# Kernel tuning notes

Hardware: AMD Instinct MI355X
Metric: run time of the kernel (lower is better)

The kernel has to match this reference:

```python
import jax, jax.numpy as jnp
import numpy as np

T, B, D, H, F, E = 2048, 2, 1024, 16, 4096, 8
HD = D // H


def layer_norm(x, g, b, eps=1e-5):
    m = x.mean(-1, keepdims=True)
    v = ((x - m) ** 2).mean(-1, keepdims=True)
    return (x - m) * jax.lax.rsqrt(v + eps) * g + b


def setup_inputs() -> dict:
    key = jax.random.key(0)
    ks = jax.random.split(key, 24)
    s = 0.02
    inp = {
        "x": jax.random.normal(ks[0], (T, B, D), jnp.float32),
        # self-attention (fairseq MultiheadAttention)
        "Wq": jax.random.normal(ks[1], (D, D), jnp.float32) * s,
        "bq": jnp.zeros((D,), jnp.float32),
        "Wk": jax.random.normal(ks[2], (D, D), jnp.float32) * s,
        "bk": jnp.zeros((D,), jnp.float32),
        "Wv": jax.random.normal(ks[3], (D, D), jnp.float32) * s,
        "bv": jnp.zeros((D,), jnp.float32),
        "Wo": jax.random.normal(ks[4], (D, D), jnp.float32) * s,
        "bo": jnp.zeros((D,), jnp.float32),
        "ln1_g": jnp.ones((D,), jnp.float32),
        "ln1_b": jnp.zeros((D,), jnp.float32),
        "ln2_g": jnp.ones((D,), jnp.float32),
        "ln2_b": jnp.zeros((D,), jnp.float32),
        # MoE: expert_centroids Linear(D -> E, bias=False) => weight [E, D]
        "cent": jax.random.normal(ks[5], (E, D), jnp.float32) * s,
        # per-expert MoESublayer params (base_sublayers=1)
        "e_ln_g": jnp.ones((E, D), jnp.float32),
        "e_ln_b": jnp.zeros((E, D), jnp.float32),
        "e_W1": jax.random.normal(ks[6], (E, D, F), jnp.float32) * s,
        "e_b1": jnp.zeros((E, F), jnp.float32),
        "e_W2": jax.random.normal(ks[7], (E, F, D), jnp.float32) * s,
        "e_b2": jnp.zeros((E, D), jnp.float32),
    }
    return inp


def reference(x, Wq, bq, Wk, bk, Wv, bv, Wo, bo, ln1_g, ln1_b, ln2_g, ln2_b,
              cent, e_ln_g, e_ln_b, e_W1, e_b1, e_W2, e_b2):
    # ---- self-attention block (pre-norm, causal) ----
    res = x  # [T,B,D]
    h = layer_norm(x, ln1_g, ln1_b)
    q = ((h @ Wq) + bq) * (HD ** -0.5)
    k = h @ Wk + bk
    v = h @ Wv + bv
    q = q.reshape(T, B, H, HD)
    k = k.reshape(T, B, H, HD)
    v = v.reshape(T, B, H, HD)
    scores = jnp.einsum('tbhd,sbhd->bhts', q, k)
    causal = jnp.tril(jnp.ones((T, T), bool))
    scores = jnp.where(causal, scores, -1e9)
    p = jax.nn.softmax(scores, axis=-1)
    a = jnp.einsum('bhts,sbhd->tbhd', p, v).reshape(T, B, D)
    x = res + (a @ Wo + bo)

    # ---- MoE block (pre-norm) ----
    res = x
    h = layer_norm(x, ln2_g, ln2_b)
    # MoELayer: transpose(0,1) then flatten -> [B*T, D] token-major by batch
    xs = h.transpose(1, 0, 2).reshape(B * T, D)
    logits = xs.astype(jnp.float32) @ cent.T  # fp32 gating, [N,E]
    assign = jnp.argmax(logits, axis=-1)      # greedy top-1 routing

    # single-device semantics: All2All identity; sort + inverse-sort cancel,
    # so out[t] = expert_{assign[t]}(xs[t]). Compute each expert densely and select.
    def sublayer(g, b, W1, b1, W2, b2):
        hh = jax.nn.relu(layer_norm(xs, g, b) @ W1 + b1)  # [N,F]
        return xs + hh @ W2 + b2                          # internal residual

    ys = jax.vmap(sublayer)(e_ln_g, e_ln_b, e_W1, e_b1, e_W2, e_b2)  # [E,N,D]
    moe_out = jnp.take_along_axis(ys, assign[None, :, None], axis=0)[0]  # [N,D]
    moe_out = moe_out.reshape(B, T, D).transpose(1, 0, 2)  # back to [T,B,D]

    return res + moe_out
```

## Files before the change

kernel.cpp:

```cpp
#include <hip/hip_runtime.h>
#include <hip/hip_bf16.h>
#include <math.h>

#define T_ 2048
#define B_ 2
#define D_ 1024
#define H_ 16
#define F_ 4096
#define E_ 8
#define N_ 4096
#define HD_ 64
#define PADROWS 5120

typedef __attribute__((ext_vector_type(8))) short short8_t;
typedef __attribute__((ext_vector_type(4))) float f32x4_t;
typedef __attribute__((ext_vector_type(16))) float f32x16_t;
typedef __attribute__((ext_vector_type(4))) unsigned u32x4_t;

__device__ __forceinline__ unsigned short f2bf(float f) {
    union { float f; unsigned u; } a; a.f = f;
    unsigned r = a.u + 0x7FFFu + ((a.u >> 16) & 1u);
    return (unsigned short)(r >> 16);
}

__device__ __forceinline__ unsigned cvtpk(float lo, float hi) {
    unsigned r;
    asm("v_cvt_pk_bf16_f32 %0, %1, %2" : "=v"(r) : "v"(lo), "v"(hi));
    return r;
}

__device__ __forceinline__ void glds16(const unsigned short* g, unsigned short* l) {
    __builtin_amdgcn_global_load_lds(
        (const __attribute__((address_space(1))) void*)g,
        (__attribute__((address_space(3))) void*)l, 16, 0, 0);
}

__device__ __forceinline__ void blockReduce2(float& a, float& b, float* sm) {
    #pragma unroll
    for (int m = 32; m; m >>= 1) { a += __shfl_xor(a, m); b += __shfl_xor(b, m); }
    const int w = threadIdx.x >> 6, l = threadIdx.x & 63;
    __syncthreads();
    if (l == 0) { sm[w] = a; sm[8 + w] = b; }
    __syncthreads();
    a = sm[0] + sm[1] + sm[2] + sm[3];
    b = sm[8] + sm[9] + sm[10] + sm[11];
}

__global__ __launch_bounds__(256) void k_transpose(const float* __restrict__ in,
                                                   unsigned short* __restrict__ out,
                                                   int R, int C) {
    __shared__ float tile[32][33];
    const int c0 = blockIdx.x * 32, r0 = blockIdx.y * 32;
    const size_t base = (size_t)blockIdx.z * R * C;
    in += base; out += base;
    const int tx = threadIdx.x & 31, ty = threadIdx.x >> 5;
    #pragma unroll
    for (int i = 0; i < 32; i += 8)
        tile[ty + i][tx] = in[(size_t)(r0 + ty + i) * C + c0 + tx];
    __syncthreads();
    #pragma unroll
    for (int i = 0; i < 32; i += 8)
        out[(size_t)(c0 + ty + i) * R + r0 + tx] = f2bf(tile[tx][ty + i]);
}

__global__ __launch_bounds__(256) void k_transpose_v(const unsigned short* __restrict__ in,
                                                     unsigned short* __restrict__ out) {
    const int bh = blockIdx.x;
    const int t0 = blockIdx.y * 128;
    const int tid = threadIdx.x;
    const int hd = tid & 63;
    const size_t ib = (size_t)bh * T_ * HD_;
    const size_t ob = (size_t)bh * HD_ * T_;
    for (int tb = tid >> 6; tb < 16; tb += 4) {
        const int t = t0 + tb * 8;
        short8_t v;
        #pragma unroll
        for (int k = 0; k < 8; ++k)
            v[k] = (short)in[ib + (size_t)(t + k) * HD_ + hd];
        *(short8_t*)(out + ob + (size_t)hd * T_ + t) = v;
    }
}

__global__ __launch_bounds__(256) void k_ln(const float* __restrict__ x,
                                            const float* __restrict__ g,
                                            const float* __restrict__ b,
                                            unsigned short* __restrict__ out) {
    __shared__ float sm[16];
    const int row = blockIdx.x, tid = threadIdx.x;
    const float4 v = *(const float4*)(x + (size_t)row * D_ + tid * 4);
    float s1 = v.x + v.y + v.z + v.w;
    float s2 = v.x * v.x + v.y * v.y + v.z * v.z + v.w * v.w;
    blockReduce2(s1, s2, sm);
    const float mean = s1 * (1.f / D_);
    const float inv  = rsqrtf(s2 * (1.f / D_) - mean * mean + 1e-5f);
    const float4 gg = *(const float4*)(g + tid * 4);
    const float4 bb = *(const float4*)(b + tid * 4);
    unsigned long long pk =
          (unsigned long long)f2bf((v.x - mean) * inv * gg.x + bb.x)
        | ((unsigned long long)f2bf((v.y - mean) * inv * gg.y + bb.y) << 16)
        | ((unsigned long long)f2bf((v.z - mean) * inv * gg.z + bb.z) << 32)
        | ((unsigned long long)f2bf((v.w - mean) * inv * gg.w + bb.w) << 48);
    *(unsigned long long*)(out + (size_t)row * D_ + tid * 4) = pk;
}

__device__ __forceinline__ void gemm_core(const unsigned short* ap0, const unsigned short* ap1,
                                          const unsigned short* bp0, const unsigned short* bp1,
                                          int K, unsigned short* Als, unsigned short* Bls,
                                          f32x4_t (&acc)[4][4]) {
    const int tid = threadIdx.x, w = tid >> 6, l = tid & 63;
    const int wm = (w >> 1) * 64, wn = (w & 1) * 64;
    const int fr = l & 15, fg = (l >> 4) * 8;
    f32x4_t z4 = {0.f, 0.f, 0.f, 0.f};
    #pragma unroll
    for (int m = 0; m < 4; m++)
        #pragma unroll
        for (int n = 0; n < 4; n++) acc[m][n] = z4;
    glds16(ap0, Als + w * 512);
    glds16(ap1, Als + (w + 4) * 512);
    glds16(bp0, Bls + w * 512);
    glds16(bp1, Bls + (w + 4) * 512);
    ap0 += 32; ap1 += 32; bp0 += 32; bp1 += 32;
    asm volatile("s_waitcnt vmcnt(0)" ::: "memory");
    __syncthreads();
    const int nk = K >> 5;
    #pragma unroll 2
    for (int kt = 0; kt < nk; ++kt) {
        const unsigned cur = (kt & 1) ? 4096u : 0u;
        const unsigned nxt = cur ^ 4096u;
        if (kt + 1 < nk) {
            glds16(ap0, Als + nxt + w * 512);
            glds16(ap1, Als + nxt + (w + 4) * 512);
            glds16(bp0, Bls + nxt + w * 512);
            glds16(bp1, Bls + nxt + (w + 4) * 512);
            ap0 += 32; ap1 += 32; bp0 += 32; bp1 += 32;
        }
        short8_t a[4], b[4];
        #pragma unroll
        for (int m = 0; m < 4; m++) a[m] = *(const short8_t*)(Als + cur + (wm + m * 16 + fr) * 32 + fg);
        #pragma unroll
        for (int n = 0; n < 4; n++) b[n] = *(const short8_t*)(Bls + cur + (wn + n * 16 + fr) * 32 + fg);
        #pragma unroll
        for (int m = 0; m < 4; m++)
            #pragma unroll
            for (int n = 0; n < 4; n++)
                acc[m][n] = __builtin_amdgcn_mfma_f32_16x16x32_bf16(a[m], b[n], acc[m][n], 0, 0, 0);
        __syncthreads();
    }
}

__global__ __launch_bounds__(256) void k_gemm_qkv(
    const unsigned short* __restrict__ A, const unsigned short* __restrict__ BT,
    const float* __restrict__ bq, const float* __restrict__ bk, const float* __restrict__ bv,
    unsigned short* __restrict__ Qb, unsigned short* __restrict__ Kb, unsigned short* __restrict__ Vb) {
    __shared__ unsigned short Als[8192], Bls[8192];
    const int tid = threadIdx.x, w = tid >> 6, l = tid & 63;
    const int col0 = blockIdx.x * 128, row0 = blockIdx.y * 128;
    const int r0s = w * 16 + (l >> 2), r1s = 64 + w * 16 + (l >> 2), cs = (l & 3) * 8;
    const unsigned short* ap0 = A + (size_t)(row0 + r0s) * D_ + cs;
    const unsigned short* ap1 = A + (size_t)(row0 + r1s) * D_ + cs;
    const unsigned short* bp0 = BT + (size_t)(col0 + r0s) * D_ + cs;
    const unsigned short* bp1 = BT + (size_t)(col0 + r1s) * D_ + cs;
    f32x4_t acc[4][4];
    gemm_core(ap0, ap1, bp0, bp1, D_, Als, Bls, acc);
    const int wm = (w >> 1) * 64, wn = (w & 1) * 64, fr = l & 15, fg4 = l >> 4;
    #pragma unroll
    for (int n = 0; n < 4; n++) {
        const int gcol = col0 + wn + n * 16 + fr;
        const int which = gcol >> 10, dc = gcol & 1023;
        const float bias = which == 0 ? bq[dc] : (which == 1 ? bk[dc] : bv[dc]);
        unsigned short* dst = which == 0 ? Qb : (which == 1 ? Kb : Vb);
        const int hh = dc >> 6, hd = dc & 63;
        #pragma unroll
        for (int m = 0; m < 4; m++)
            #pragma unroll
            for (int rr = 0; rr < 4; rr++) {
                const int grow = row0 + wm + m * 16 + fg4 * 4 + rr;
                float v = acc[m][n][rr] + bias;
                if (which == 0) v *= 0.1803368801111204f;
                const int t = grow >> 1, bb = grow & 1;
                dst[((size_t)(bb * H_ + hh) * T_ + t) * HD_ + hd] = f2bf(v);
            }
    }
}

__global__ __launch_bounds__(256) void k_attn(const unsigned short* __restrict__ Qb,
                                              const unsigned short* __restrict__ Kb,
                                              const unsigned short* __restrict__ Vt,
                                              unsigned short* __restrict__ aout) {
    __shared__ unsigned short Kl[2][4096];
    __shared__ unsigned short Vl[2][4096];
    const int id = blockIdx.x;
    const int qt = (id < 256) ? (15 - (id & 15)) : (id & 15);
    const int bh = (id >> 4) & 31;
    const int tid = threadIdx.x, w = tid >> 6, l = tid & 63;
    const int q5 = l & 31, hi = l >> 5, l7 = l & 7;
    const int row0 = w * 8 + (l >> 3);
    const int swz = ((l & 7) ^ (l >> 3)) * 8;
    const size_t base = (size_t)bh * T_ * HD_;
    const unsigned short* Qp = Qb + base;
    const unsigned short* kps = Kb + base + (size_t)row0 * HD_ + swz;
    const unsigned short* vps = Vt + base + (size_t)row0 * T_ + swz;
    const int qw0 = qt * 128 + w * 32;
    const int q = qw0 + q5;

    short8_t aq[4];
    #pragma unroll
    for (int khd = 0; khd < 4; ++khd)
        aq[khd] = *(const short8_t*)(Qp + (size_t)q * HD_ + khd * 16 + hi * 8);

    f32x16_t accO0, accO1;
    #pragma unroll
    for (int i = 0; i < 16; ++i) { accO0[i] = 0.f; accO1[i] = 0.f; }
    float mrun = -1e30f, lrun = 0.f;

    const int niter = (qt + 1) * 2;

    glds16(kps,            &Kl[0][w * 512]);
    glds16(kps + 32 * HD_, &Kl[0][2048 + w * 512]);
    glds16(vps,            &Vl[0][w * 512]);
    glds16(vps + 32 * T_,  &Vl[0][2048 + w * 512]);
    asm volatile("s_waitcnt vmcnt(0)" ::: "memory");
    __syncthreads();

    for (int it = 0; it < niter; ++it) {
        const int cur = it & 1;
        const int s0 = it * 64;
        if (it + 1 < niter) {
            const size_t ko = (size_t)(it + 1) * 64 * HD_;
            const int vo = (it + 1) * 64;
            glds16(kps + ko,            &Kl[cur ^ 1][w * 512]);
            glds16(kps + ko + 32 * HD_, &Kl[cur ^ 1][2048 + w * 512]);
            glds16(vps + vo,            &Vl[cur ^ 1][w * 512]);
            glds16(vps + vo + 32 * T_,  &Vl[cur ^ 1][2048 + w * 512]);
        }
        if (s0 <= qw0 + 31) {
            const unsigned short* KT = Kl[cur];
            const unsigned short* VT = Vl[cur];

            f32x16_t st0, st1;
            #pragma unroll
            for (int i = 0; i < 16; ++i) { st0[i] = 0.f; st1[i] = 0.f; }
            #pragma unroll
            for (int khd = 0; khd < 4; ++khd) {
                const int cb = (khd * 16 + hi * 8) ^ (l7 * 8);
                const short8_t k0 = *(const short8_t*)(KT + q5 * 64 + cb);
                const short8_t k1 = *(const short8_t*)(KT + (32 + q5) * 64 + cb);
                st0 = __builtin_amdgcn_mfma_f32_32x32x16_bf16(k0, aq[khd], st0, 0, 0, 0);
                st1 = __builtin_amdgcn_mfma_f32_32x32x16_bf16(k1, aq[khd], st1, 0, 0, 0);
            }

            const bool domask = (s0 + 63 > qw0);
            float pmax = -3e38f;
            #pragma unroll
            for (int r = 0; r < 16; ++r) {
                float v0 = st0[r], v1 = st1[r];
                if (domask) {
                    const int kv0 = s0 + (r & 3) + 8 * (r >> 2) + 4 * hi;
                    if (kv0 > q)      v0 = -1e30f;
                    if (kv0 + 32 > q) v1 = -1e30f;
                }
                st0[r] = v0; st1[r] = v1;
                pmax = fmaxf(pmax, fmaxf(v0, v1));
            }
            pmax = fmaxf(pmax, __shfl_xor(pmax, 32));
            const float mnew = fmaxf(mrun, pmax);
            const float scl = exp2f(mrun - mnew);
            float pt0[16], pt1[16];
            float rs = 0.f;
            #pragma unroll
            for (int r = 0; r < 16; ++r) {
                pt0[r] = exp2f(st0[r] - mnew);
                pt1[r] = exp2f(st1[r] - mnew);
                rs += pt0[r] + pt1[r];
            }
            rs += __shfl_xor(rs, 32);
            lrun = lrun * scl + rs;
            mrun = mnew;
            #pragma unroll
            for (int i = 0; i < 16; ++i) { accO0[i] *= scl; accO1[i] *= scl; }

            unsigned Wp[2][4][2];
            #pragma unroll
            for (int b = 0; b < 4; ++b) {
                Wp[0][b][0] = cvtpk(pt0[4 * b + 0], pt0[4 * b + 1]);
                Wp[0][b][1] = cvtpk(pt0[4 * b + 2], pt0[4 * b + 3]);
                Wp[1][b][0] = cvtpk(pt1[4 * b + 0], pt1[4 * b + 1]);
                Wp[1][b][1] = cvtpk(pt1[4 * b + 2], pt1[4 * b + 3]);
            }

            #pragma unroll
            for (int ks = 0; ks < 4; ++ks) {
                const int t = ks >> 1, b0 = (ks & 1) * 2;
                const unsigned ownA0 = Wp[t][b0][0],     ownA1 = Wp[t][b0][1];
                const unsigned ownB0 = Wp[t][b0 + 1][0], ownB1 = Wp[t][b0 + 1][1];
                const unsigned send0 = hi ? ownA0 : ownB0;
                const unsigned send1 = hi ? ownA1 : ownB1;
                const unsigned recv0 = __shfl_xor(send0, 32);
                const unsigned recv1 = __shfl_xor(send1, 32);
                u32x4_t wds;
                wds[0] = hi ? recv0 : ownA0;
                wds[1] = hi ? recv1 : ownA1;
                wds[2] = hi ? ownB0 : recv0;
                wds[3] = hi ? ownB1 : recv1;
                const short8_t pfrag = __builtin_bit_cast(short8_t, wds);
                const int cb = (ks * 16 + hi * 8) ^ (l7 * 8);
                const short8_t v0 = *(const short8_t*)(VT + q5 * 64 + cb);
                const short8_t v1 = *(const short8_t*)(VT + (32 + q5) * 64 + cb);
                accO0 = __builtin_amdgcn_mfma_f32_32x32x16_bf16(v0, pfrag, accO0, 0, 0, 0);
                accO1 = __builtin_amdgcn_mfma_f32_32x32x16_bf16(v1, pfrag, accO1, 0, 0, 0);
            }
        }
        asm volatile("s_waitcnt vmcnt(0)" ::: "memory");
        __syncthreads();
    }

    const float linv = 1.f / lrun;
    const int bidx = bh >> 4, hidx = bh & 15;
    unsigned short* orow = aout + (size_t)(q * B_ + bidx) * D_ + hidx * 64;
    #pragma unroll
    for (int g = 0; g < 4; ++g) {
        const int hd0 = 8 * g + 4 * hi;
        unsigned long long pk0 =
              (unsigned long long)f2bf(accO0[4 * g + 0] * linv)
            | ((unsigned long long)f2bf(accO0[4 * g + 1] * linv) << 16)
            | ((unsigned long long)f2bf(accO0[4 * g + 2] * linv) << 32)
            | ((unsigned long long)f2bf(accO0[4 * g + 3] * linv) << 48);
        *(unsigned long long*)(orow + hd0) = pk0;
        unsigned long long pk1 =
              (unsigned long long)f2bf(accO1[4 * g + 0] * linv)
            | ((unsigned long long)f2bf(accO1[4 * g + 1] * linv) << 16)
            | ((unsigned long long)f2bf(accO1[4 * g + 2] * linv) << 32)
            | ((unsigned long long)f2bf(accO1[4 * g + 3] * linv) << 48);
        *(unsigned long long*)(orow + 32 + hd0) = pk1;
    }
}

__global__ __launch_bounds__(256) void k_gemm_o(
    const unsigned short* __restrict__ A, const unsigned short* __restrict__ BT,
    const float* __restrict__ bo, const float* __restrict__ xin, float* __restrict__ x2) {
    __shared__ unsigned short Als[8192], Bls[8192];
    const int tid = threadIdx.x, w = tid >> 6, l = tid & 63;
    const int col0 = blockIdx.x * 128, row0 = blockIdx.y * 128;
    const int r0s = w * 16 + (l >> 2), r1s = 64 + w * 16 + (l >> 2), cs = (l & 3) * 8;
    const unsigned short* ap0 = A + (size_t)(row0 + r0s) * D_ + cs;
    const unsigned short* ap1 = A + (size_t)(row0 + r1s) * D_ + cs;
    const unsigned short* bp0 = BT + (size_t)(col0 + r0s) * D_ + cs;
    const unsigned short* bp1 = BT + (size_t)(col0 + r1s) * D_ + cs;
    f32x4_t acc[4][4];
    gemm_core(ap0, ap1, bp0, bp1, D_, Als, Bls, acc);
    const int wm = (w >> 1) * 64, wn = (w & 1) * 64, fr = l & 15, fg4 = l >> 4;
    #pragma unroll
    for (int n = 0; n < 4; n++) {
        const int gcol = col0 + wn + n * 16 + fr;
        const float bias = bo[gcol];
        #pragma unroll
        for (int m = 0; m < 4; m++)
            #pragma unroll
            for (int rr = 0; rr < 4; rr++) {
                const int grow = row0 + wm + m * 16 + fg4 * 4 + rr;
                const size_t idx = (size_t)grow * D_ + gcol;
                x2[idx] = xin[idx] + acc[m][n][rr] + bias;
            }
    }
}

__global__ __launch_bounds__(256) void k_ln2_gate(
    float* __restrict__ x2, const float* __restrict__ g2, const float* __restrict__ b2,
    const float* __restrict__ cent, const float* __restrict__ eg, const float* __restrict__ eb,
    unsigned short* __restrict__ z, int* __restrict__ assign, int* __restrict__ counts) {
    __shared__ float sm[48];
    const int row = blockIdx.x, tid = threadIdx.x;
    const int w = tid >> 6, l = tid & 63;
    float* xr = x2 + (size_t)row * D_;
    const float4 v = *(const float4*)(xr + tid * 4);
    float s1 = v.x + v.y + v.z + v.w;
    float s2 = v.x * v.x + v.y * v.y + v.z * v.z + v.w * v.w;
    blockReduce2(s1, s2, sm);
    const float mean = s1 * (1.f / D_);
    const float inv  = rsqrtf(s2 * (1.f / D_) - mean * mean + 1e-5f);
    const float4 gg = *(const float4*)(g2 + tid * 4), bb = *(const float4*)(b2 + tid * 4);
    float4 u;
    u.x = (v.x - mean) * inv * gg.x + bb.x;
    u.y = (v.y - mean) * inv * gg.y + bb.y;
    u.z = (v.z - mean) * inv * gg.z + bb.z;
    u.w = (v.w - mean) * inv * gg.w + bb.w;
    float p[E_];
    #pragma unroll
    for (int e = 0; e < E_; e++) {
        const float4 c = *(const float4*)(cent + (size_t)e * D_ + tid * 4);
        p[e] = u.x * c.x + u.y * c.y + u.z * c.z + u.w * c.w;
    }
    #pragma unroll
    for (int m = 32; m; m >>= 1)
        #pragma unroll
        for (int e = 0; e < E_; e++) p[e] += __shfl_xor(p[e], m);
    __syncthreads();
    if (l == 0) {
        #pragma unroll
        for (int e = 0; e < E_; e++) sm[16 + e * 4 + w] = p[e];
    }
    __syncthreads();
    int best = 0; float bl = -1e30f;
    #pragma unroll
    for (int e = 0; e < E_; e++) {
        const float le = sm[16 + e * 4] + sm[16 + e * 4 + 1] + sm[16 + e * 4 + 2] + sm[16 + e * 4 + 3];
        if (le > bl) { bl = le; best = e; }
    }
    float t1 = u.x + u.y + u.z + u.w;
    float t2 = u.x * u.x + u.y * u.y + u.z * u.z + u.w * u.w;
    blockReduce2(t1, t2, sm);
    const float m2   = t1 * (1.f / D_);
    const float inv2 = rsqrtf(t2 * (1.f / D_) - m2 * m2 + 1e-5f);
    const float4 egv = *(const float4*)(eg + (size_t)best * D_ + tid * 4);
    const float4 ebv = *(const float4*)(eb + (size_t)best * D_ + tid * 4);
    unsigned long long pk =
          (unsigned long long)f2bf((u.x - m2) * inv2 * egv.x + ebv.x)
        | ((unsigned long long)f2bf((u.y - m2) * inv2 * egv.y + ebv.y) << 16)
        | ((unsigned long long)f2bf((u.z - m2) * inv2 * egv.z + ebv.z) << 32)
        | ((unsigned long long)f2bf((u.w - m2) * inv2 * egv.w + ebv.w) << 48);
    *(unsigned long long*)(z + (size_t)row * D_ + tid * 4) = pk;
    float4 xu; xu.x = v.x + u.x; xu.y = v.y + u.y; xu.z = v.z + u.z; xu.w = v.w + u.w;
    *(float4*)(xr + tid * 4) = xu;
    if (tid == 0) { assign[row] = best; atomicAdd(&counts[best], 1); }
}

__global__ void k_init(int* counts, int* cursor, int* perm) {
    const int t = threadIdx.x;
    if (t < E_) { counts[t] = 0; cursor[t] = 0; }
    for (int i = t; i < PADROWS; i += 256) perm[i] = -1;
}

__global__ void k_offsets(const int* counts, int* pad_off) {
    if (threadIdx.x == 0) {
        int o = 0; pad_off[0] = 0;
        for (int e = 0; e < E_; e++) { o += ((counts[e] + 127) >> 7) << 7; pad_off[e + 1] = o; }
    }
}

__global__ void k_scatter(const int* assign, const int* pad_off, int* cursor, int* perm) {
    const int r = blockIdx.x * 256 + threadIdx.x;
    if (r >= N_) return;
    const int e = assign[r];
    const int pos = pad_off[e] + atomicAdd(&cursor[e], 1);
    perm[pos] = r;
}

__global__ __launch_bounds__(256) void k_gemm_e1(
    const unsigned short* __restrict__ z, const unsigned short* __restrict__ W1T,
    const float* __restrict__ eb1, const int* __restrict__ pad_off,
    const int* __restrict__ perm, unsigned short* __restrict__ Y1) {
    __shared__ unsigned short Als[8192], Bls[8192];
    const int tid = threadIdx.x, w = tid >> 6, l = tid & 63;
    const int col0 = blockIdx.x * 128, row0 = blockIdx.y * 128;
    if (row0 >= pad_off[E_]) return;
    int e = 0;
    while (row0 >= pad_off[e + 1]) e++;
    const int r0s = w * 16 + (l >> 2), r1s = 64 + w * 16 + (l >> 2), cs = (l & 3) * 8;
    int pr0 = perm[row0 + r0s]; if (pr0 < 0) pr0 = 0;
    int pr1 = perm[row0 + r1s]; if (pr1 < 0) pr1 = 0;
    const unsigned short* ap0 = z + (size_t)pr0 * D_ + cs;
    const unsigned short* ap1 = z + (size_t)pr1 * D_ + cs;
    const unsigned short* BTe = W1T + (size_t)e * F_ * D_;
    const unsigned short* bp0 = BTe + (size_t)(col0 + r0s) * D_ + cs;
    const unsigned short* bp1 = BTe + (size_t)(col0 + r1s) * D_ + cs;
    f32x4_t acc[4][4];
    gemm_core(ap0, ap1, bp0, bp1, D_, Als, Bls, acc);
    const float* b1e = eb1 + (size_t)e * F_;
    const int wm = (w >> 1) * 64, wn = (w & 1) * 64, fr = l & 15, fg4 = l >> 4;
    #pragma unroll
    for (int n = 0; n < 4; n++) {
        const int gcol = col0 + wn + n * 16 + fr;
        const float bias = b1e[gcol];
        #pragma unroll
        for (int m = 0; m < 4; m++)
            #pragma unroll
            for (int rr = 0; rr < 4; rr++) {
                const int grow = row0 + wm + m * 16 + fg4 * 4 + rr;
                Y1[(size_t)grow * F_ + gcol] = f2bf(fmaxf(acc[m][n][rr] + bias, 0.f));
            }
    }
}

__global__ __launch_bounds__(256) void k_gemm_e2(
    const unsigned short* __restrict__ Y1, const unsigned short* __restrict__ W2T,
    const float* __restrict__ eb2, const int* __restrict__ pad_off,
    const int* __restrict__ perm, const float* __restrict__ x2u, float* __restrict__ out) {
    __shared__ unsigned short Als[8192], Bls[8192];
    const int tid = threadIdx.x, w = tid >> 6, l = tid & 63;
    const int col0 = blockIdx.x * 128, row0 = blockIdx.y * 128;
    if (row0 >= pad_off[E_]) return;
    int e = 0;
    while (row0 >= pad_off[e + 1]) e++;
    const int r0s = w * 16 + (l >> 2), r1s = 64 + w * 16 + (l >> 2), cs = (l & 3) * 8;
    const unsigned short* ap0 = Y1 + (size_t)(row0 + r0s) * F_ + cs;
    const unsigned short* ap1 = Y1 + (size_t)(row0 + r1s) * F_ + cs;
    const unsigned short* BTe = W2T + (size_t)e * D_ * F_;
    const unsigned short* bp0 = BTe + (size_t)(col0 + r0s) * F_ + cs;
    const unsigned short* bp1 = BTe + (size_t)(col0 + r1s) * F_ + cs;
    f32x4_t acc[4][4];
    gemm_core(ap0, ap1, bp0, bp1, F_, Als, Bls, acc);
    const float* b2e = eb2 + (size_t)e * D_;
    const int wm = (w >> 1) * 64, wn = (w & 1) * 64, fr = l & 15, fg4 = l >> 4;
    #pragma unroll
    for (int n = 0; n < 4; n++) {
        const int gcol = col0 + wn + n * 16 + fr;
        const float bias = b2e[gcol];
        #pragma unroll
        for (int m = 0; m < 4; m++)
            #pragma unroll
            for (int rr = 0; rr < 4; rr++) {
                const int grow = row0 + wm + m * 16 + fg4 * 4 + rr;
                const int rdst = perm[grow];
                if (rdst >= 0) {
                    const size_t idx = (size_t)rdst * D_ + gcol;
                    out[idx] = x2u[idx] + acc[m][n][rr] + bias;
                }
            }
    }
}

extern "C" void kernel_launch(void* const* d_in, const int* in_sizes, int n_in,
                              void* d_out, int out_size, void* d_ws, size_t ws_size,
                              hipStream_t stream) {
    const float* x    = (const float*)d_in[0];
    const float* Wq   = (const float*)d_in[1];
    const float* bq   = (const float*)d_in[2];
    const float* Wk   = (const float*)d_in[3];
    const float* bk   = (const float*)d_in[4];
    const float* Wv   = (const float*)d_in[5];
    const float* bv   = (const float*)d_in[6];
    const float* Wo   = (const float*)d_in[7];
    const float* bo   = (const float*)d_in[8];
    const float* ln1g = (const float*)d_in[9];
    const float* ln1b = (const float*)d_in[10];
    const float* ln2g = (const float*)d_in[11];
    const float* ln2b = (const float*)d_in[12];
    const float* cent = (const float*)d_in[13];
    const float* egw  = (const float*)d_in[14];
    const float* ebw  = (const float*)d_in[15];
    const float* eW1  = (const float*)d_in[16];
    const float* eb1  = (const float*)d_in[17];
    const float* eW2  = (const float*)d_in[18];
    const float* eb2  = (const float*)d_in[19];
    float* out = (float*)d_out;

    char* W = (char*)d_ws;
    unsigned short* WqkvT = (unsigned short*)(W);
    unsigned short* WoT   = (unsigned short*)(W + 6291456);
    unsigned short* Qb    = (unsigned short*)(W + 8388608);
    unsigned short* Kb    = (unsigned short*)(W + 16777216);
    unsigned short* Vb    = (unsigned short*)(W + 25165824);
    unsigned short* aout  = (unsigned short*)(W + 33554432);
    unsigned short* Y1    = (unsigned short*)(W);
    unsigned short* W1T   = (unsigned short*)(W + 41943040);
    unsigned short* W2T   = (unsigned short*)(W + 109051904);
    unsigned short* h1z   = (unsigned short*)(W + 176160768);
    float*          x2    = (float*)(W + 184549376);
    unsigned short* Vt    = (unsigned short*)(W + 201326592);
    int*            assign= (int*)(W + 209715200);
    int*            perm  = (int*)(W + 209731584);
    int*            counts= (int*)(W + 209752064);
    int*            cursor= (int*)(W + 209752192);
    int*            pad_off=(int*)(W + 209752320);

    k_transpose<<<dim3(32, 32, 1), 256, 0, stream>>>(Wq, WqkvT,               1024, 1024);
    k_transpose<<<dim3(32, 32, 1), 256, 0, stream>>>(Wk, WqkvT + 1024 * 1024, 1024, 1024);
    k_transpose<<<dim3(32, 32, 1), 256, 0, stream>>>(Wv, WqkvT + 2048 * 1024, 1024, 1024);
    k_transpose<<<dim3(32, 32, 1), 256, 0, stream>>>(Wo, WoT,                 1024, 1024);
    k_transpose<<<dim3(128, 32, 8), 256, 0, stream>>>(eW1, W1T, 1024, 4096);
    k_transpose<<<dim3(32, 128, 8), 256, 0, stream>>>(eW2, W2T, 4096, 1024);

    k_init<<<1, 256, 0, stream>>>(counts, cursor, perm);
    k_ln<<<N_, 256, 0, stream>>>(x, ln1g, ln1b, h1z);
    k_gemm_qkv<<<dim3(24, 32), 256, 0, stream>>>(h1z, WqkvT, bq, bk, bv, Qb, Kb, Vb);
    k_transpose_v<<<dim3(32, 16), 256, 0, stream>>>(Vb, Vt);
    k_attn<<<dim3(512), 256, 0, stream>>>(Qb, Kb, Vt, aout);
    k_gemm_o<<<dim3(8, 32), 256, 0, stream>>>(aout, WoT, bo, x, x2);
    k_ln2_gate<<<N_, 256, 0, stream>>>(x2, ln2g, ln2b, cent, egw, ebw, h1z, assign, counts);
    k_offsets<<<1, 64, 0, stream>>>(counts, pad_off);
    k_scatter<<<16, 256, 0, stream>>>(assign, pad_off, cursor, perm);
    k_gemm_e1<<<dim3(32, 40), 256, 0, stream>>>(h1z, W1T, eb1, pad_off, perm, Y1);
    k_gemm_e2<<<dim3(8, 40), 256, 0, stream>>>(Y1, W2T, eb2, pad_off, perm, x2, out);
}
```

Before: 536.2 us.

## Split-K the output-projection and expert-down GEMMs with atomic accumulation

The O-projection and second expert GEMM now split their K dimension in two across a grid z axis and accumulate partial results with atomicAdd. Two new elementwise kernels pre-initialize the destinations with residual plus bias. The aim is more blocks for better CU occupancy on the small-grid GEMMs. In exchange it adds atomic traffic, extra init passes over the output, and non-deterministic summation order.

```diff
diff --git a/kernel.cpp b/kernel.cpp
--- a/kernel.cpp
+++ b/kernel.cpp
@@ -101,6 +101,30 @@
         | ((unsigned long long)f2bf((v.z - mean) * inv * gg.z + bb.z) << 32)
         | ((unsigned long long)f2bf((v.w - mean) * inv * gg.w + bb.w) << 48);
     *(unsigned long long*)(out + (size_t)row * D_ + tid * 4) = pk;
+}
+
+__global__ __launch_bounds__(256) void k_init_x2(const float* __restrict__ x,
+                                                 const float* __restrict__ bo,
+                                                 float* __restrict__ x2) {
+    const int row = blockIdx.x, tid = threadIdx.x;
+    const size_t idx = (size_t)row * D_ + tid * 4;
+    const float4 v = *(const float4*)(x + idx);
+    const float4 b = *(const float4*)(bo + tid * 4);
+    float4 o; o.x = v.x + b.x; o.y = v.y + b.y; o.z = v.z + b.z; o.w = v.w + b.w;
+    *(float4*)(x2 + idx) = o;
+}
+
+__global__ __launch_bounds__(256) void k_init_out(const float* __restrict__ x2u,
+                                                  const float* __restrict__ eb2,
+                                                  const int* __restrict__ assign,
+                                                  float* __restrict__ out) {
+    const int row = blockIdx.x, tid = threadIdx.x;
+    const int e = assign[row];
+    const size_t idx = (size_t)row * D_ + tid * 4;
+    const float4 v = *(const float4*)(x2u + idx);
+    const float4 b = *(const float4*)(eb2 + (size_t)e * D_ + tid * 4);
+    float4 o; o.x = v.x + b.x; o.y = v.y + b.y; o.z = v.z + b.z; o.w = v.w + b.w;
+    *(float4*)(out + idx) = o;
 }
 
 __device__ __forceinline__ void gemm_core(const unsigned short* ap0, const unsigned short* ap1,
@@ -337,29 +361,28 @@
 
 __global__ __launch_bounds__(256) void k_gemm_o(
     const unsigned short* __restrict__ A, const unsigned short* __restrict__ BT,
-    const float* __restrict__ bo, const float* __restrict__ xin, float* __restrict__ x2) {
+    float* __restrict__ x2) {
     __shared__ unsigned short Als[8192], Bls[8192];
     const int tid = threadIdx.x, w = tid >> 6, l = tid & 63;
-    const int col0 = blockIdx.x * 128, row0 = blockIdx.y * 128;
+    const int row0 = blockIdx.x * 128, col0 = blockIdx.y * 128;
+    const int kc = blockIdx.z * 512;
     const int r0s = w * 16 + (l >> 2), r1s = 64 + w * 16 + (l >> 2), cs = (l & 3) * 8;
-    const unsigned short* ap0 = A + (size_t)(row0 + r0s) * D_ + cs;
-    const unsigned short* ap1 = A + (size_t)(row0 + r1s) * D_ + cs;
-    const unsigned short* bp0 = BT + (size_t)(col0 + r0s) * D_ + cs;
-    const unsigned short* bp1 = BT + (size_t)(col0 + r1s) * D_ + cs;
+    const unsigned short* ap0 = A + (size_t)(row0 + r0s) * D_ + kc + cs;
+    const unsigned short* ap1 = A + (size_t)(row0 + r1s) * D_ + kc + cs;
+    const unsigned short* bp0 = BT + (size_t)(col0 + r0s) * D_ + kc + cs;
+    const unsigned short* bp1 = BT + (size_t)(col0 + r1s) * D_ + kc + cs;
     f32x4_t acc[4][4];
-    gemm_core(ap0, ap1, bp0, bp1, D_, Als, Bls, acc);
+    gemm_core(ap0, ap1, bp0, bp1, 512, Als, Bls, acc);
     const int wm = (w >> 1) * 64, wn = (w & 1) * 64, fr = l & 15, fg4 = l >> 4;
     #pragma unroll
     for (int n = 0; n < 4; n++) {
         const int gcol = col0 + wn + n * 16 + fr;
-        const float bias = bo[gcol];
         #pragma unroll
         for (int m = 0; m < 4; m++)
             #pragma unroll
             for (int rr = 0; rr < 4; rr++) {
                 const int grow = row0 + wm + m * 16 + fg4 * 4 + rr;
-                const size_t idx = (size_t)grow * D_ + gcol;
-                x2[idx] = xin[idx] + acc[m][n][rr] + bias;
+                atomicAdd(&x2[(size_t)grow * D_ + gcol], acc[m][n][rr]);
             }
     }
 }
@@ -483,38 +506,35 @@
 
 __global__ __launch_bounds__(256) void k_gemm_e2(
     const unsigned short* __restrict__ Y1, const unsigned short* __restrict__ W2T,
-    const float* __restrict__ eb2, const int* __restrict__ pad_off,
-    const int* __restrict__ perm, const float* __restrict__ x2u, float* __restrict__ out) {
+    const int* __restrict__ pad_off, const int* __restrict__ perm,
+    float* __restrict__ out) {
     __shared__ unsigned short Als[8192], Bls[8192];
     const int tid = threadIdx.x, w = tid >> 6, l = tid & 63;
-    const int col0 = blockIdx.x * 128, row0 = blockIdx.y * 128;
+    const int row0 = blockIdx.x * 128, col0 = blockIdx.y * 128;
+    const int kc = blockIdx.z * 2048;
     if (row0 >= pad_off[E_]) return;
     int e = 0;
     while (row0 >= pad_off[e + 1]) e++;
     const int r0s = w * 16 + (l >> 2), r1s = 64 + w * 16 + (l >> 2), cs = (l & 3) * 8;
-    const unsigned short* ap0 = Y1 + (size_t)(row0 + r0s) * F_ + cs;
-    const unsigned short* ap1 = Y1 + (size_t)(row0 + r1s) * F_ + cs;
+    const unsigned short* ap0 = Y1 + (size_t)(row0 + r0s) * F_ + kc + cs;
+    const unsigned short* ap1 = Y1 + (size_t)(row0 + r1s) * F_ + kc + cs;
     const unsigned short* BTe = W2T + (size_t)e * D_ * F_;
-    const unsigned short* bp0 = BTe + (size_t)(col0 + r0s) * F_ + cs;
-    const unsigned short* bp1 = BTe + (size_t)(col0 + r1s) * F_ + cs;
+    const unsigned short* bp0 = BTe + (size_t)(col0 + r0s) * F_ + kc + cs;
+    const unsigned short* bp1 = BTe + (size_t)(col0 + r1s) * F_ + kc + cs;
     f32x4_t acc[4][4];
-    gemm_core(ap0, ap1, bp0, bp1, F_, Als, Bls, acc);
-    const float* b2e = eb2 + (size_t)e * D_;
+    gemm_core(ap0, ap1, bp0, bp1, 2048, Als, Bls, acc);
     const int wm = (w >> 1) * 64, wn = (w & 1) * 64, fr = l & 15, fg4 = l >> 4;
     #pragma unroll
     for (int n = 0; n < 4; n++) {
         const int gcol = col0 + wn + n * 16 + fr;
-        const float bias = b2e[gcol];
         #pragma unroll
         for (int m = 0; m < 4; m++)
             #pragma unroll
             for (int rr = 0; rr < 4; rr++) {
                 const int grow = row0 + wm + m * 16 + fg4 * 4 + rr;
                 const int rdst = perm[grow];
-                if (rdst >= 0) {
-                    const size_t idx = (size_t)rdst * D_ + gcol;
-                    out[idx] = x2u[idx] + acc[m][n][rr] + bias;
-                }
+                if (rdst >= 0)
+                    atomicAdd(&out[(size_t)rdst * D_ + gcol], acc[m][n][rr]);
             }
     }
 }
@@ -572,13 +592,15 @@
 
     k_init<<<1, 256, 0, stream>>>(counts, cursor, perm);
     k_ln<<<N_, 256, 0, stream>>>(x, ln1g, ln1b, h1z);
+    k_init_x2<<<N_, 256, 0, stream>>>(x, bo, x2);
     k_gemm_qkv<<<dim3(24, 32), 256, 0, stream>>>(h1z, WqkvT, bq, bk, bv, Qb, Kb, Vb);
     k_transpose_v<<<dim3(32, 16), 256, 0, stream>>>(Vb, Vt);
     k_attn<<<dim3(512), 256, 0, stream>>>(Qb, Kb, Vt, aout);
-    k_gemm_o<<<dim3(8, 32), 256, 0, stream>>>(aout, WoT, bo, x, x2);
+    k_gemm_o<<<dim3(32, 8, 2), 256, 0, stream>>>(aout, WoT, x2);
     k_ln2_gate<<<N_, 256, 0, stream>>>(x2, ln2g, ln2b, cent, egw, ebw, h1z, assign, counts);
     k_offsets<<<1, 64, 0, stream>>>(counts, pad_off);
     k_scatter<<<16, 256, 0, stream>>>(assign, pad_off, cursor, perm);
+    k_init_out<<<N_, 256, 0, stream>>>(x2, eb2, assign, out);
     k_gemm_e1<<<dim3(32, 40), 256, 0, stream>>>(h1z, W1T, eb1, pad_off, perm, Y1);
-    k_gemm_e2<<<dim3(8, 40), 256, 0, stream>>>(Y1, W2T, eb2, pad_off, perm, x2, out);
-}
+    k_gemm_e2<<<dim3(40, 8, 2), 256, 0, stream>>>(Y1, W2T, pad_off, perm, out);
+}
```

After: 510.3 us. 4.8% less time.
